# Kernel tuning notes

Measured on AMD Instinct MI355X. Metric: run time of the kernel, lower is better.

Reference implementation:

```python
import jax, jax.numpy as jnp
import numpy as np

N = 100000      # nodes
E = 1000000     # edges
IN_DIM = 128
OUT_DIM = 64
K = 4
ALPHA = 0.5
LAMBD = 1.0


def setup_inputs() -> dict:
    key = jax.random.key(0)
    k1, k2, k3, k4 = jax.random.split(key, 4)
    features = jax.random.normal(k1, (N, IN_DIM), dtype=jnp.float32)
    # xavier_uniform for Linear weight [out, in]
    limit = float(np.sqrt(6.0 / (IN_DIM + OUT_DIM)))
    W = jax.random.uniform(k2, (OUT_DIM, IN_DIM), dtype=jnp.float32,
                           minval=-limit, maxval=limit)
    b = jnp.zeros((OUT_DIM,), dtype=jnp.float32)
    src = jax.random.randint(k3, (E,), 0, N, dtype=jnp.int32)
    dst = jax.random.randint(k4, (E,), 0, N, dtype=jnp.int32)
    return {"features": features, "W": W, "b": b, "src": src, "dst": dst}


def reference(features, W, b, src, dst):
    # in-degrees = number of edges entering each node (dst occurrences)
    degs = jax.ops.segment_sum(jnp.ones((E,), jnp.float32), dst, num_segments=N)
    norm_lambd_1 = (LAMBD * degs + 1.0) ** (-1.0)          # [N]
    norm05 = jnp.sqrt(degs + 1.0)[:, None]                 # [N,1]
    norm_05 = jax.lax.rsqrt(degs + 1.0)[:, None]           # [N,1]
    norm_lambd_1 = norm_lambd_1[:, None]                   # [N,1]

    h = features @ W.T + b                                 # [N, OUT]
    h_pre = h
    h_initial = h * norm_lambd_1

    def step(carry, _):
        h, h_pre = carry
        hh = h * norm_05                                   # D^{-1/2} scaling
        agg = jax.ops.segment_sum(hh[src], dst, num_segments=N)  # SpMM (copy_u, sum)
        h2 = agg * norm_lambd_1 * norm05
        hn = ALPHA * LAMBD * h2 + (1.0 - ALPHA) * h_pre + ALPHA * h_initial
        return (hn, hn), None

    (h, _), _ = jax.lax.scan(step, (h, h_pre), None, length=K)
    return h
```

## Files before the change

kernel.cpp:

```cpp
#include <hip/hip_runtime.h>

#define NN 100000
#define NE 1000000
#define IND 128
#define OUTD 64
#define GM 64
#define MAXDEG 64
#define GEMM_BLKS ((NN + GM - 1) / GM)
#define BUCK_BLKS ((NE + 255) / 256)
#define FUSE_GRPS 782

typedef float vf4 __attribute__((ext_vector_type(4)));
typedef short bf8 __attribute__((ext_vector_type(8)));
typedef unsigned int u32;

__device__ __forceinline__ unsigned short f2bf(float f) {
    unsigned int x = __float_as_uint(f);
    return (unsigned short)((x + 0x7fffu + ((x >> 16) & 1u)) >> 16);
}
__device__ __forceinline__ unsigned int packbf(float a, float b) {
    return (unsigned int)f2bf(a) | ((unsigned int)f2bf(b) << 16);
}
__device__ __forceinline__ float lo16(unsigned int u) { return __uint_as_float(u << 16); }
__device__ __forceinline__ float hi16(unsigned int u) { return __uint_as_float(u & 0xffff0000u); }


__global__ __launch_bounds__(256) void k_build_gemm(
        const float* __restrict__ feat, const float* __restrict__ W,
        const float* __restrict__ bias,
        unsigned short* __restrict__ h016,
        const int* __restrict__ src, const int* __restrict__ dst,
        int* __restrict__ cnt, int* __restrict__ colidx) {
    int g = blockIdx.x / 7, m = blockIdx.x % 7;
    if (m >= 2) {
        int b = g * 5 + (m - 2);
        if (b < BUCK_BLKS) {
            int e = b * 256 + threadIdx.x;
            if (e < NE) {
                int d = dst[e];
                int rank = atomicAdd(&cnt[d], 1);
                if (rank < MAXDEG) colidx[d * MAXDEG + rank] = src[e];
            }
        }
        return;
    }
    int gb = g * 2 + m;
    if (gb >= GEMM_BLKS) return;

    __shared__ u32 Fl[GM * 64];
    __shared__ u32 Wl[OUTD * 64];
    int t = threadIdx.x;
    int n0 = gb * GM;

#pragma unroll
    for (int i = 0; i < 4; ++i) {
        int c = t + i * 256;
        int row = c >> 4, kc8 = c & 15;
        vf4 x0 = ((const vf4*)W)[row * 32 + kc8 * 2];
        vf4 x1 = ((const vf4*)W)[row * 32 + kc8 * 2 + 1];
        uint4 p;
        p.x = packbf(x0.x, x0.y); p.y = packbf(x0.z, x0.w);
        p.z = packbf(x1.x, x1.y); p.w = packbf(x1.z, x1.w);
        *(uint4*)((char*)Wl + row * 256 + ((kc8 ^ (row & 7)) << 4)) = p;
    }
#pragma unroll
    for (int i = 0; i < 4; ++i) {
        int c = t + i * 256;
        int row = c >> 4, kc8 = c & 15;
        int n = n0 + row;
        vf4 x0 = (vf4)(0.0f), x1 = (vf4)(0.0f);
        if (n < NN) {
            x0 = __builtin_nontemporal_load(&((const vf4*)feat)[n * 32 + kc8 * 2]);
            x1 = __builtin_nontemporal_load(&((const vf4*)feat)[n * 32 + kc8 * 2 + 1]);
        }
        uint4 p;
        p.x = packbf(x0.x, x0.y); p.y = packbf(x0.z, x0.w);
        p.z = packbf(x1.x, x1.y); p.w = packbf(x1.z, x1.w);
        *(uint4*)((char*)Fl + row * 256 + ((kc8 ^ (row & 7)) << 4)) = p;
    }
    __syncthreads();

    int lane = t & 63, wv = t >> 6;
    int mrow = lane & 15, q = lane >> 4;
    vf4 acc[4];
#pragma unroll
    for (int ct = 0; ct < 4; ++ct) acc[ct] = (vf4)(0.0f);

    int arow = wv * 16 + mrow;
#pragma unroll
    for (int kc = 0; kc < 4; ++kc) {
        bf8 a = *(const bf8*)((const char*)Fl + arow * 256 +
                              (((kc * 4 + q) ^ (arow & 7)) << 4));
#pragma unroll
        for (int ct = 0; ct < 4; ++ct) {
            int ch = ct * 16 + mrow;
            bf8 b = *(const bf8*)((const char*)Wl + ch * 256 +
                                  (((kc * 4 + q) ^ (ch & 7)) << 4));
            acc[ct] = __builtin_amdgcn_mfma_f32_16x16x32_bf16(a, b, acc[ct], 0, 0, 0);
        }
    }

    float bv[4];
#pragma unroll
    for (int ct = 0; ct < 4; ++ct) bv[ct] = bias[ct * 16 + mrow];

#pragma unroll
    for (int reg = 0; reg < 4; ++reg) {
        int n = n0 + wv * 16 + q * 4 + reg;
        if (n < NN) {
#pragma unroll
            for (int ct = 0; ct < 4; ++ct) {
                int ch = ct * 16 + mrow;
                h016[(size_t)n * OUTD + ch] = f2bf(acc[ct][reg] + bv[ct]);
            }
        }
    }
}


template<bool FIRST, bool FINAL>
__global__ __launch_bounds__(256) void k_gather16(
        float* __restrict__ hn, unsigned short* __restrict__ gn16,
        const unsigned short* __restrict__ st16,
        const unsigned short* __restrict__ h016,
        const int* __restrict__ cnt, const int* __restrict__ colidx) {
    int t = blockIdx.x * 256 + threadIdx.x;
    int wave = t >> 6;
    int lane = t & 63;
    int q  = lane >> 3;
    int c8 = lane & 7;
    int v = wave * 8 + q;
    bool valid = v < NN;
    int vc = valid ? v : NN - 1;
    int dc = cnt[vc];
    float rv = rsqrtf((float)dc + 1.0f);
    int deg = min(dc, MAXDEG);
    if (!valid) deg = 0;
    int beg = vc * MAXDEG;
    int md = deg;
    md = max(md, __shfl_xor(md, 8, 64));
    md = max(md, __shfl_xor(md, 16, 64));
    md = max(md, __shfl_xor(md, 32, 64));

    float a0 = 0.f, a1 = 0.f, a2 = 0.f, a3 = 0.f;
    float a4 = 0.f, a5 = 0.f, a6 = 0.f, a7 = 0.f;
    int nb = (md + 7) >> 3;
    for (int b = 0; b < nb; ++b) {
        int kb = b * 8;
        int sj[8]; int cj[8]; uint4 u[8];
#pragma unroll
        for (int j = 0; j < 8; ++j) {
            int k = kb + j;
            sj[j] = (k < deg) ? colidx[beg + k] : 0;
        }
#pragma unroll
        for (int j = 0; j < 8; ++j) {
            u[j]  = *(const uint4*)(st16 + (size_t)sj[j] * OUTD + 8 * c8);
            cj[j] = cnt[sj[j]];
        }
#pragma unroll
        for (int j = 0; j < 8; ++j) {
            if (kb + j < deg) {
                float rs = rsqrtf((float)cj[j] + 1.0f);
                a0 = fmaf(rs, lo16(u[j].x), a0); a1 = fmaf(rs, hi16(u[j].x), a1);
                a2 = fmaf(rs, lo16(u[j].y), a2); a3 = fmaf(rs, hi16(u[j].y), a3);
                a4 = fmaf(rs, lo16(u[j].z), a4); a5 = fmaf(rs, hi16(u[j].z), a5);
                a6 = fmaf(rs, lo16(u[j].w), a6); a7 = fmaf(rs, hi16(u[j].w), a7);
            }
        }
    }

    if (valid) {
        float hr  = 0.5f * rv;
        float s2h = 0.5f * rv * rv;
        size_t base = (size_t)v * OUTD + 8 * c8;
        uint4 us = *(const uint4*)(st16 + base);
        uint4 u0 = FIRST ? us : *(const uint4*)(h016 + base);
        float o0 = fmaf(hr, a0, fmaf(s2h, lo16(u0.x), 0.5f * lo16(us.x)));
        float o1 = fmaf(hr, a1, fmaf(s2h, hi16(u0.x), 0.5f * hi16(us.x)));
        float o2 = fmaf(hr, a2, fmaf(s2h, lo16(u0.y), 0.5f * lo16(us.y)));
        float o3 = fmaf(hr, a3, fmaf(s2h, hi16(u0.y), 0.5f * hi16(us.y)));
        float o4 = fmaf(hr, a4, fmaf(s2h, lo16(u0.z), 0.5f * lo16(us.z)));
        float o5 = fmaf(hr, a5, fmaf(s2h, hi16(u0.z), 0.5f * hi16(us.z)));
        float o6 = fmaf(hr, a6, fmaf(s2h, lo16(u0.w), 0.5f * lo16(us.w)));
        float o7 = fmaf(hr, a7, fmaf(s2h, hi16(u0.w), 0.5f * hi16(us.w)));
        if (FINAL) {
            vf4 w0 = { o0, o1, o2, o3 };
            vf4 w1 = { o4, o5, o6, o7 };
            __builtin_nontemporal_store(w0, (vf4*)(hn + base));
            __builtin_nontemporal_store(w1, (vf4*)(hn + base + 4));
        } else {
            uint4 p;
            p.x = packbf(o0, o1);
            p.y = packbf(o2, o3);
            p.z = packbf(o4, o5);
            p.w = packbf(o6, o7);
            *(uint4*)(gn16 + base) = p;
        }
    }
}


extern "C" void kernel_launch(void* const* d_in, const int* in_sizes, int n_in,
                              void* d_out, int out_size, void* d_ws, size_t ws_size,
                              hipStream_t stream) {
    const float* feat = (const float*)d_in[0];
    const float* W    = (const float*)d_in[1];
    const float* bias = (const float*)d_in[2];
    const int*   src  = (const int*)d_in[3];
    const int*   dst  = (const int*)d_in[4];

    char* ws = (char*)d_ws;
    int*            cnt    = (int*)(ws + 0);
    int*            colidx = (int*)(ws + 400000);
    unsigned short* h016   = (unsigned short*)(ws + 26000000);
    unsigned short* hA     = (unsigned short*)(ws + 38800000);
    unsigned short* hB     = (unsigned short*)(ws + 51600000);

    hipMemsetAsync(cnt, 0, NN * sizeof(int), stream);

    k_build_gemm<<<FUSE_GRPS * 7, 256, 0, stream>>>(
        feat, W, bias, h016, src, dst, cnt, colidx);

    int gth_blocks = (NN + 31) / 32;
    k_gather16<true,  false><<<gth_blocks, 256, 0, stream>>>(
        nullptr, hA, h016, h016, cnt, colidx);
    k_gather16<false, false><<<gth_blocks, 256, 0, stream>>>(
        nullptr, hB, hA, h016, cnt, colidx);
    k_gather16<false, false><<<gth_blocks, 256, 0, stream>>>(
        nullptr, hA, hB, h016, cnt, colidx);
    k_gather16<false, true><<<gth_blocks, 256, 0, stream>>>(
        (float*)d_out, nullptr, hA, h016, cnt, colidx);
}
```

Before: 178.8 us.

## Store pre-scaled intermediate features to drop per-neighbor degree lookups

Intermediate iterations now store h scaled by the node's rsqrt(deg+1), so later gather passes sum neighbor rows directly without loading cnt[src] and computing rsqrt per edge. The epilogue is rewritten to undo the scaling for the residual term. Column indices are read as two 16-byte vector loads instead of eight scalar loads, and the per-wave max-degree shuffle is replaced with a per-lane loop bound. The vector loads can read up to seven padding slots past the degree inside the fixed 64-slot row, and keeping the stored values pre-scaled in bf16 slightly changes rounding.

```diff
diff --git a/kernel.cpp b/kernel.cpp
--- a/kernel.cpp
+++ b/kernel.cpp
@@ -28,7 +28,7 @@
 __global__ __launch_bounds__(256) void k_build_gemm(
         const float* __restrict__ feat, const float* __restrict__ W,
         const float* __restrict__ bias,
-        unsigned short* __restrict__ h016,
+        unsigned short* __restrict__ hraw16,
         const int* __restrict__ src, const int* __restrict__ dst,
         int* __restrict__ cnt, int* __restrict__ colidx) {
     int g = blockIdx.x / 7, m = blockIdx.x % 7;
@@ -111,7 +111,7 @@
 #pragma unroll
             for (int ct = 0; ct < 4; ++ct) {
                 int ch = ct * 16 + mrow;
-                h016[(size_t)n * OUTD + ch] = f2bf(acc[ct][reg] + bv[ct]);
+                hraw16[(size_t)n * OUTD + ch] = f2bf(acc[ct][reg] + bv[ct]);
             }
         }
     }
@@ -122,7 +122,7 @@
 __global__ __launch_bounds__(256) void k_gather16(
         float* __restrict__ hn, unsigned short* __restrict__ gn16,
         const unsigned short* __restrict__ st16,
-        const unsigned short* __restrict__ h016,
+        const unsigned short* __restrict__ hraw16,
         const int* __restrict__ cnt, const int* __restrict__ colidx) {
     int t = blockIdx.x * 256 + threadIdx.x;
     int wave = t >> 6;
@@ -134,56 +134,80 @@
     int vc = valid ? v : NN - 1;
     int dc = cnt[vc];
     float rv = rsqrtf((float)dc + 1.0f);
-    int deg = min(dc, MAXDEG);
-    if (!valid) deg = 0;
+    int deg = valid ? min(dc, MAXDEG) : 0;
     int beg = vc * MAXDEG;
-    int md = deg;
-    md = max(md, __shfl_xor(md, 8, 64));
-    md = max(md, __shfl_xor(md, 16, 64));
-    md = max(md, __shfl_xor(md, 32, 64));
 
     float a0 = 0.f, a1 = 0.f, a2 = 0.f, a3 = 0.f;
     float a4 = 0.f, a5 = 0.f, a6 = 0.f, a7 = 0.f;
-    int nb = (md + 7) >> 3;
+    int nb = (deg + 7) >> 3;
     for (int b = 0; b < nb; ++b) {
         int kb = b * 8;
-        int sj[8]; int cj[8]; uint4 u[8];
+        uint4 ci0 = *(const uint4*)(colidx + beg + kb);
+        uint4 ci1 = *(const uint4*)(colidx + beg + kb + 4);
+        int sj[8];
+        sj[0] = (kb + 0 < deg) ? (int)ci0.x : 0;
+        sj[1] = (kb + 1 < deg) ? (int)ci0.y : 0;
+        sj[2] = (kb + 2 < deg) ? (int)ci0.z : 0;
+        sj[3] = (kb + 3 < deg) ? (int)ci0.w : 0;
+        sj[4] = (kb + 4 < deg) ? (int)ci1.x : 0;
+        sj[5] = (kb + 5 < deg) ? (int)ci1.y : 0;
+        sj[6] = (kb + 6 < deg) ? (int)ci1.z : 0;
+        sj[7] = (kb + 7 < deg) ? (int)ci1.w : 0;
+        uint4 u[8];
+        int cj[8];
 #pragma unroll
         for (int j = 0; j < 8; ++j) {
-            int k = kb + j;
-            sj[j] = (k < deg) ? colidx[beg + k] : 0;
-        }
-#pragma unroll
-        for (int j = 0; j < 8; ++j) {
-            u[j]  = *(const uint4*)(st16 + (size_t)sj[j] * OUTD + 8 * c8);
-            cj[j] = cnt[sj[j]];
+            u[j] = *(const uint4*)(st16 + (size_t)sj[j] * OUTD + 8 * c8);
+            if (FIRST) cj[j] = cnt[sj[j]];
         }
 #pragma unroll
         for (int j = 0; j < 8; ++j) {
             if (kb + j < deg) {
-                float rs = rsqrtf((float)cj[j] + 1.0f);
-                a0 = fmaf(rs, lo16(u[j].x), a0); a1 = fmaf(rs, hi16(u[j].x), a1);
-                a2 = fmaf(rs, lo16(u[j].y), a2); a3 = fmaf(rs, hi16(u[j].y), a3);
-                a4 = fmaf(rs, lo16(u[j].z), a4); a5 = fmaf(rs, hi16(u[j].z), a5);
-                a6 = fmaf(rs, lo16(u[j].w), a6); a7 = fmaf(rs, hi16(u[j].w), a7);
+                float rs = FIRST ? rsqrtf((float)cj[j] + 1.0f) : 1.0f;
+                if (FIRST) {
+                    a0 = fmaf(rs, lo16(u[j].x), a0); a1 = fmaf(rs, hi16(u[j].x), a1);
+                    a2 = fmaf(rs, lo16(u[j].y), a2); a3 = fmaf(rs, hi16(u[j].y), a3);
+                    a4 = fmaf(rs, lo16(u[j].z), a4); a5 = fmaf(rs, hi16(u[j].z), a5);
+                    a6 = fmaf(rs, lo16(u[j].w), a6); a7 = fmaf(rs, hi16(u[j].w), a7);
+                } else {
+                    a0 += lo16(u[j].x); a1 += hi16(u[j].x);
+                    a2 += lo16(u[j].y); a3 += hi16(u[j].y);
+                    a4 += lo16(u[j].z); a5 += hi16(u[j].z);
+                    a6 += lo16(u[j].w); a7 += hi16(u[j].w);
+                }
             }
         }
     }
 
     if (valid) {
-        float hr  = 0.5f * rv;
-        float s2h = 0.5f * rv * rv;
+        float hr = 0.5f * rv;
+        float s2 = 0.5f * rv * rv;
         size_t base = (size_t)v * OUTD + 8 * c8;
-        uint4 us = *(const uint4*)(st16 + base);
-        uint4 u0 = FIRST ? us : *(const uint4*)(h016 + base);
-        float o0 = fmaf(hr, a0, fmaf(s2h, lo16(u0.x), 0.5f * lo16(us.x)));
-        float o1 = fmaf(hr, a1, fmaf(s2h, hi16(u0.x), 0.5f * hi16(us.x)));
-        float o2 = fmaf(hr, a2, fmaf(s2h, lo16(u0.y), 0.5f * lo16(us.y)));
-        float o3 = fmaf(hr, a3, fmaf(s2h, hi16(u0.y), 0.5f * hi16(us.y)));
-        float o4 = fmaf(hr, a4, fmaf(s2h, lo16(u0.z), 0.5f * lo16(us.z)));
-        float o5 = fmaf(hr, a5, fmaf(s2h, hi16(u0.z), 0.5f * hi16(us.z)));
-        float o6 = fmaf(hr, a6, fmaf(s2h, lo16(u0.w), 0.5f * lo16(us.w)));
-        float o7 = fmaf(hr, a7, fmaf(s2h, hi16(u0.w), 0.5f * hi16(us.w)));
+        float o0, o1, o2, o3, o4, o5, o6, o7;
+        if (FIRST) {
+            float cs = 0.5f + s2;
+            uint4 h0 = *(const uint4*)(st16 + base);
+            o0 = fmaf(hr, a0, cs * lo16(h0.x));
+            o1 = fmaf(hr, a1, cs * hi16(h0.x));
+            o2 = fmaf(hr, a2, cs * lo16(h0.y));
+            o3 = fmaf(hr, a3, cs * hi16(h0.y));
+            o4 = fmaf(hr, a4, cs * lo16(h0.z));
+            o5 = fmaf(hr, a5, cs * hi16(h0.z));
+            o6 = fmaf(hr, a6, cs * lo16(h0.w));
+            o7 = fmaf(hr, a7, cs * hi16(h0.w));
+        } else {
+            float ir2 = 0.5f / rv;
+            uint4 gs = *(const uint4*)(st16 + base);
+            uint4 h0 = *(const uint4*)(hraw16 + base);
+            o0 = fmaf(hr, a0, fmaf(lo16(gs.x), ir2, s2 * lo16(h0.x)));
+            o1 = fmaf(hr, a1, fmaf(hi16(gs.x), ir2, s2 * hi16(h0.x)));
+            o2 = fmaf(hr, a2, fmaf(lo16(gs.y), ir2, s2 * lo16(h0.y)));
+            o3 = fmaf(hr, a3, fmaf(hi16(gs.y), ir2, s2 * hi16(h0.y)));
+            o4 = fmaf(hr, a4, fmaf(lo16(gs.z), ir2, s2 * lo16(h0.z)));
+            o5 = fmaf(hr, a5, fmaf(hi16(gs.z), ir2, s2 * hi16(h0.z)));
+            o6 = fmaf(hr, a6, fmaf(lo16(gs.w), ir2, s2 * lo16(h0.w)));
+            o7 = fmaf(hr, a7, fmaf(hi16(gs.w), ir2, s2 * hi16(h0.w)));
+        }
         if (FINAL) {
             vf4 w0 = { o0, o1, o2, o3 };
             vf4 w1 = { o4, o5, o6, o7 };
@@ -191,10 +215,10 @@
             __builtin_nontemporal_store(w1, (vf4*)(hn + base + 4));
         } else {
             uint4 p;
-            p.x = packbf(o0, o1);
-            p.y = packbf(o2, o3);
-            p.z = packbf(o4, o5);
-            p.w = packbf(o6, o7);
+            p.x = packbf(o0 * rv, o1 * rv);
+            p.y = packbf(o2 * rv, o3 * rv);
+            p.z = packbf(o4 * rv, o5 * rv);
+            p.w = packbf(o6 * rv, o7 * rv);
             *(uint4*)(gn16 + base) = p;
         }
     }
@@ -213,22 +237,22 @@
     char* ws = (char*)d_ws;
     int*            cnt    = (int*)(ws + 0);
     int*            colidx = (int*)(ws + 400000);
-    unsigned short* h016   = (unsigned short*)(ws + 26000000);
-    unsigned short* hA     = (unsigned short*)(ws + 38800000);
-    unsigned short* hB     = (unsigned short*)(ws + 51600000);
+    unsigned short* hraw16 = (unsigned short*)(ws + 26000000);
+    unsigned short* g16A   = (unsigned short*)(ws + 38800000);
+    unsigned short* g16B   = (unsigned short*)(ws + 51600000);
 
     hipMemsetAsync(cnt, 0, NN * sizeof(int), stream);
 
     k_build_gemm<<<FUSE_GRPS * 7, 256, 0, stream>>>(
-        feat, W, bias, h016, src, dst, cnt, colidx);
+        feat, W, bias, hraw16, src, dst, cnt, colidx);
 
     int gth_blocks = (NN + 31) / 32;
     k_gather16<true,  false><<<gth_blocks, 256, 0, stream>>>(
-        nullptr, hA, h016, h016, cnt, colidx);
+        nullptr, g16A, hraw16, hraw16, cnt, colidx);
     k_gather16<false, false><<<gth_blocks, 256, 0, stream>>>(
-        nullptr, hB, hA, h016, cnt, colidx);
+        nullptr, g16B, g16A, hraw16, cnt, colidx);
     k_gather16<false, false><<<gth_blocks, 256, 0, stream>>>(
-        nullptr, hA, hB, h016, cnt, colidx);
+        nullptr, g16A, g16B, hraw16, cnt, colidx);
     k_gather16<false, true><<<gth_blocks, 256, 0, stream>>>(
-        (float*)d_out, nullptr, hA, h016, cnt, colidx);
-}
+        (float*)d_out, nullptr, g16A, hraw16, cnt, colidx);
+}
```

New measurement: 161.9 us. 9.4% less time.
